# Kernel optimization log

Hardware: AMD Instinct MI355X
Metric: run time of the kernel (lower is better)

## Reference

```python
import jax, jax.numpy as jnp
import numpy as np

NUM_CODES = 1024
CODE_DIM = 256
COMMIT_W = 0.25
EPS = 1e-5
ENT_LO, ENT_HI = 0.5, 0.9
ENT_W = 0.1
VAR_FLOOR = 0.05
VAR_W = 1e-3
DECORR_W = 1e-3


def setup_inputs() -> dict:
    key = jax.random.key(0)
    k1, k2, k3 = jax.random.split(key, 3)
    inputs = jax.random.normal(k1, (16, 2048, CODE_DIM), dtype=jnp.float32)
    weight = jax.random.normal(k2, (NUM_CODES, CODE_DIM), dtype=jnp.float32) * 0.1
    usage_counts = jax.random.uniform(k3, (NUM_CODES,), dtype=jnp.float32)
    return {"inputs": inputs, "weight": weight, "usage_counts": usage_counts}


def reference(inputs, weight, usage_counts):
    K, D = weight.shape
    flat = inputs.reshape(-1, D)  # [N, D]
    # squared euclidean distances [N, K]
    dist = (flat ** 2).sum(axis=1, keepdims=True) - 2.0 * flat @ weight.T + (weight ** 2).sum(axis=1)
    idx = jnp.argmin(dist, axis=1)  # [N]
    quant = weight[idx].reshape(inputs.shape)

    commitment_loss = COMMIT_W * jnp.mean((jax.lax.stop_gradient(quant) - inputs) ** 2)
    # straight-through estimator
    quant_ste = inputs + jax.lax.stop_gradient(quant - inputs)

    # usage entropy regularizer
    probs = usage_counts + EPS
    probs = probs / jnp.maximum(probs.sum(), EPS * K)
    usage_entropy = -jnp.sum(probs * jnp.log(probs + EPS)) / np.log(float(K)).astype(np.float32)
    gap = jnp.where(usage_entropy < ENT_LO, ENT_LO - usage_entropy,
                    jnp.where(usage_entropy > ENT_HI, usage_entropy - ENT_HI, 0.0))
    entropy_loss = ENT_W * gap ** 2

    # variance floor penalty on codebook
    variance = jnp.var(weight, axis=0)
    variance_loss = VAR_W * jnp.mean(jax.nn.relu(VAR_FLOOR - variance))

    # decorrelation penalty
    wc = weight - weight.mean(axis=0, keepdims=True)
    cov = wc.T @ wc / float(K)  # [D, D]
    off_diag = cov - jnp.diag(jnp.diag(cov))
    decorrelation_loss = DECORR_W * jnp.mean(off_diag ** 2)

    total_loss = commitment_loss + entropy_loss + variance_loss + decorrelation_loss
    indices = idx.reshape(inputs.shape[:-1])
    return (quant_ste, indices, total_loss, commitment_loss, entropy_loss,
            variance_loss, decorrelation_loss, usage_entropy)
```

## Files before the change

### kernel.cpp

```cpp
#include <hip/hip_runtime.h>
#include <math.h>

#define DIMS   256
#define KCODES 1024
#define NTOT   32768
#define TAU    4.0e-4f

typedef __bf16 bf16x8 __attribute__((ext_vector_type(8)));
typedef float  f32x4  __attribute__((ext_vector_type(4)));

#define WS_COMMIT   0
#define WS_FLAGCNT  1
#define WS_DECORR   2
#define WS_COLSUM   16
#define WS_COLSQ    272
#define WS_WSQ      1024
#define WS_XSQ      2048
#define WS_FLAGS    34816
#define WS_CAND1    67584
#define WS_CAND2    329728
#define WS_CANDI    591872
#define WS_WP       854016

#define OUT_Q    0
#define OUT_IDX  8388608
#define OUT_SCAL 8421376


__global__ __launch_bounds__(256) void prep_kernel(const float* __restrict__ X,
                                                   const float* __restrict__ W,
                                                   __bf16* __restrict__ Xp,
                                                   __bf16* __restrict__ Wp2,
                                                   float* ws) {
  int b = blockIdx.x;
  int tid = threadIdx.x;
  if (b < 1056) {
    bool isW = b >= 1024;
    const float* src = isW ? W : X;
    __bf16* dst = isW ? Wp2 : Xp;
    int sqoff = isW ? WS_WSQ : WS_XSQ;
    int bb = isW ? b - 1024 : b;
    int kt = tid >> 5, mtl = (tid >> 4) & 1, lc = tid & 15;
    int row = bb * 32 + mtl * 16 + lc;
    int bt = row >> 7, c = row & 127;
    int wv = c >> 6, t = (c >> 4) & 3;
    size_t hibase = ((((size_t)(bt * 8 + kt) * 2 + wv) * 4 + t) * 2) * 512;
    const float* s = src + (size_t)row * DIMS + kt * 32;
    float sq = 0.f;
    #pragma unroll
    for (int kq = 0; kq < 4; kq++) {
      float4 u = *(const float4*)(s + kq * 8);
      float4 v = *(const float4*)(s + kq * 8 + 4);
      float f[8] = {u.x, u.y, u.z, u.w, v.x, v.y, v.z, v.w};
      bf16x8 hi, lo;
      #pragma unroll
      for (int e = 0; e < 8; e++) {
        __bf16 h = (__bf16)f[e];
        hi[e] = h;
        lo[e] = (__bf16)(f[e] - (float)h);
        sq = fmaf(f[e], f[e], sq);
      }
      size_t off = (size_t)(kq * 16 + lc) * 8;
      *(bf16x8*)&dst[hibase + off] = hi;
      *(bf16x8*)&dst[hibase + 512 + off] = lo;
    }
    atomicAdd(&ws[sqoff + row], sq);
  } else if (b < 1064) {
    int d = tid;
    int r0 = (b - 1056) * 128;
    float s = 0.f, sq = 0.f;
    #pragma unroll 8
    for (int k = 0; k < 128; k++) {
      float v = W[(size_t)(r0 + k) * DIMS + d];
      s += v;
      sq = fmaf(v, v, sq);
    }
    atomicAdd(&ws[WS_COLSUM + d], s);
    atomicAdd(&ws[WS_COLSQ + d], sq);
  } else {
    __shared__ float wi_s[2][KCODES];
    __shared__ float red2[256];
    __shared__ float mi_s[2];
    __shared__ float red[4];
    int i0 = (b - 1064) * 2;
    int rr = tid >> 1, cc = tid & 1;
    #pragma unroll
    for (int q = 0; q < 8; q++) {
      int row = q * 128 + rr;
      wi_s[cc][row] = W[(size_t)row * DIMS + i0 + cc];
    }
    __syncthreads();
    float pm = 0.f;
    #pragma unroll
    for (int q = 0; q < 8; q++) pm += wi_s[cc][rr * 8 + q];
    red2[tid] = pm;
    __syncthreads();
    if (tid < 2) {
      float s = 0.f;
      for (int k = tid; k < 256; k += 2) s += red2[k];
      mi_s[tid] = s * (1.0f / 1024.0f);
    }
    int j = tid;
    float a0 = 0.f, a1 = 0.f, sj = 0.f;
    for (int k = 0; k < KCODES; k += 4) {
      #pragma unroll
      for (int u = 0; u < 4; u++) {
        float wj = W[(size_t)(k + u) * DIMS + j];
        a0 = fmaf(wi_s[0][k + u], wj, a0);
        a1 = fmaf(wi_s[1][k + u], wj, a1);
        sj += wj;
      }
    }
    __syncthreads();
    const float inv = 1.0f / 1024.0f;
    float mj = sj * inv;
    float v = 0.f;
    float c0 = a0 * inv - mi_s[0] * mj;
    if (i0 != j) v = fmaf(c0, c0, v);
    float c1 = a1 * inv - mi_s[1] * mj;
    if (i0 + 1 != j) v = fmaf(c1, c1, v);
    #pragma unroll
    for (int m = 32; m >= 1; m >>= 1) v += __shfl_xor(v, m);
    if ((j & 63) == 0) red[j >> 6] = v;
    __syncthreads();
    if (j == 0) atomicAdd(&ws[WS_DECORR], (red[0] + red[1]) + (red[2] + red[3]));
  }
}

__device__ __forceinline__ void stage16(const __bf16* g, __bf16* l) {
  __builtin_amdgcn_global_load_lds(
      (const __attribute__((address_space(1))) void*)g,
      (__attribute__((address_space(3))) void*)l, 16, 0, 0);
}

#define STAGE_PIECE(T, J) do {                                                    \
    int _s = (T) % 3;                                                             \
    if ((J) < 4) {                                                                \
      int _c = (J) >> 1, _h = (J) & 1;                                            \
      stage16(Xp + (size_t)((2 * bm + _c) * 8 + (T)) * 8192 + _h * 4096 + tid * 8,\
              buf + _s * 24576 + _c * 8192 + _h * 4096 + tid * 8);                \
    } else {                                                                      \
      int _h = (J) - 4;                                                           \
      stage16(Wp2 + (size_t)(bn * 8 + (T)) * 8192 + _h * 4096 + tid * 8,          \
              buf + _s * 24576 + 16384 + _h * 4096 + tid * 8);                    \
    }                                                                             \
  } while (0)

__global__ __launch_bounds__(512, 2) void pass1_kernel(const __bf16* __restrict__ Xp,
                                                       const __bf16* __restrict__ Wp2,
                                                       float* ws) {
  __shared__ __align__(16) __bf16 buf[73728];
  __shared__ float wsqs[128];
  __shared__ float d1L[512];
  __shared__ float d2L[512];
  __shared__ int   i1L[512];

  int tid = threadIdx.x;
  int lane = tid & 63, wave = tid >> 6;
  int wm = wave >> 1, wn = wave & 1;
  int quad = lane >> 4, col = lane & 15;
  int l = blockIdx.x;
  int swz = (l & 7) * 128 + (l >> 3);
  int bm = swz >> 3;
  int bn = swz & 7;
  int cb = bn * 128;

  f32x4 acc[4][4];
  #pragma unroll
  for (int i = 0; i < 4; i++)
    #pragma unroll
    for (int j = 0; j < 4; j++) acc[i][j] = (f32x4){0.f, 0.f, 0.f, 0.f};

  wsqs[tid & 127] = ws[WS_WSQ + cb + (tid & 127)];
  asm volatile("" ::: "memory");

  #pragma unroll
  for (int t = 0; t < 3; t++) {
    STAGE_PIECE(t, 0); STAGE_PIECE(t, 1); STAGE_PIECE(t, 2);
    STAGE_PIECE(t, 3); STAGE_PIECE(t, 4); STAGE_PIECE(t, 5);
  }
  asm volatile("s_waitcnt vmcnt(12)" ::: "memory");
  __builtin_amdgcn_s_barrier();

  #pragma unroll
  for (int kt = 0; kt < 8; kt++) {
    const __bf16* bsl = buf + (kt % 3) * 24576 + lane * 8;
    bf16x8 Bf[4][2];
    #pragma unroll
    for (int p = 0; p < 4; p++) {
      bf16x8 A0 = *(const bf16x8*)(bsl + wm * 4096 + (p * 2 + 0) * 512);
      bf16x8 A1 = *(const bf16x8*)(bsl + wm * 4096 + (p * 2 + 1) * 512);
      if (p == 0) {
        #pragma unroll
        for (int nt = 0; nt < 4; nt++) {
          Bf[nt][0] = *(const bf16x8*)(bsl + 16384 + wn * 4096 + (nt * 2 + 0) * 512);
          Bf[nt][1] = *(const bf16x8*)(bsl + 16384 + wn * 4096 + (nt * 2 + 1) * 512);
        }
      }
      if (kt + 2 < 8) {
        if (p == 0) { STAGE_PIECE(kt + 2, 0); STAGE_PIECE(kt + 2, 1); }
        if (p == 1) { STAGE_PIECE(kt + 2, 2); STAGE_PIECE(kt + 2, 3); }
        if (p == 2) { STAGE_PIECE(kt + 2, 4); }
        if (p == 3) { STAGE_PIECE(kt + 2, 5); }
      }
      if (p == 3 && kt < 7) {
        if (kt <= 5) asm volatile("s_waitcnt vmcnt(6)" ::: "memory");
        else         asm volatile("s_waitcnt vmcnt(0)" ::: "memory");
      }
      __builtin_amdgcn_s_barrier();
      asm volatile("s_waitcnt lgkmcnt(0)" ::: "memory");
      __builtin_amdgcn_sched_barrier(0);
      __builtin_amdgcn_s_setprio(1);
      #pragma unroll
      for (int nt = 0; nt < 4; nt++) {
        acc[p][nt] = __builtin_amdgcn_mfma_f32_16x16x32_bf16(A0, Bf[nt][0], acc[p][nt], 0, 0, 0);
        acc[p][nt] = __builtin_amdgcn_mfma_f32_16x16x32_bf16(A0, Bf[nt][1], acc[p][nt], 0, 0, 0);
        acc[p][nt] = __builtin_amdgcn_mfma_f32_16x16x32_bf16(A1, Bf[nt][0], acc[p][nt], 0, 0, 0);
      }
      __builtin_amdgcn_s_setprio(0);
      __builtin_amdgcn_s_barrier();
    }
  }

  #pragma unroll
  for (int mt = 0; mt < 4; mt++) {
    #pragma unroll
    for (int r = 0; r < 4; r++) {
      float d1 = 3.0e38f, d2 = 3.0e38f;
      int i1 = 0;
      #pragma unroll
      for (int nt = 0; nt < 4; nt++) {
        int lc = wn * 64 + nt * 16 + col;
        float d = wsqs[lc] - 2.0f * acc[mt][nt][r];
        int g = cb + lc;
        if (d < d1) { d2 = d1; d1 = d; i1 = g; }
        else if (d < d2) d2 = d;
      }
      #pragma unroll
      for (int m = 1; m < 16; m <<= 1) {
        float od1 = __shfl_xor(d1, m);
        int oi1 = __shfl_xor(i1, m);
        float od2 = __shfl_xor(d2, m);
        if (od1 < d1 || (od1 == d1 && oi1 < i1)) {
          d2 = fminf(d1, fminf(d2, od2));
          d1 = od1; i1 = oi1;
        } else {
          d2 = fminf(od1, fminf(d2, od2));
        }
      }
      if (col == 0) {
        int lr = wm * 64 + mt * 16 + quad * 4 + r;
        d1L[lr * 2 + wn] = d1;
        d2L[lr * 2 + wn] = d2;
        i1L[lr * 2 + wn] = i1;
      }
    }
  }
  __syncthreads();
  if (tid < 256) {
    float a1 = d1L[tid * 2], a2 = d2L[tid * 2];
    int ai = i1L[tid * 2];
    float b1 = d1L[tid * 2 + 1], b2 = d2L[tid * 2 + 1];
    int bi = i1L[tid * 2 + 1];
    float m1, m2; int mi;
    if (b1 < a1 || (b1 == a1 && bi < ai)) { m1 = b1; mi = bi; m2 = fminf(a1, b2); }
    else { m1 = a1; mi = ai; m2 = fminf(b1, a2); }
    int o = bn * NTOT + bm * 256 + tid;
    ws[WS_CAND1 + o] = m1;
    ws[WS_CAND2 + o] = m2;
    ((int*)ws)[WS_CANDI + o] = mi;
  }
}

__global__ __launch_bounds__(256) void pass2_kernel(const float* __restrict__ W,
                                                    float* __restrict__ outQ,
                                                    float* __restrict__ outIdx, float* ws) {
  __shared__ int idx_s[256];
  int tid = threadIdx.x;
  int row = blockIdx.x * 256 + tid;
  const float* c1 = ws + WS_CAND1;
  const float* c2 = ws + WS_CAND2;
  const int* ci = (const int*)ws + WS_CANDI;
  float m1 = 3.0e38f, m2 = 3.0e38f;
  int mi = 0;
  #pragma unroll
  for (int b = 0; b < 8; b++) {
    int o = b * NTOT + row;
    float b1 = c1[o], b2 = c2[o];
    int bi = ci[o];
    if (b1 < m1 || (b1 == m1 && bi < mi)) { m2 = fminf(m1, b2); m1 = b1; mi = bi; }
    else { m2 = fminf(m2, b1); }
  }
  outIdx[row] = (float)mi;
  idx_s[tid] = mi;
  int* wsI = (int*)ws;
  if (m2 - m1 < TAU) {
    int p = atomicAdd(&wsI[WS_FLAGCNT], 1);
    wsI[WS_FLAGS + p] = row;
  }
  float partial = ws[WS_XSQ + row] + m1;
  #pragma unroll
  for (int m = 32; m >= 1; m >>= 1) partial += __shfl_xor(partial, m);
  if ((tid & 63) == 0) atomicAdd(&ws[WS_COMMIT], partial);
  __syncthreads();
  int wave = tid >> 6, lane = tid & 63;
  int rowBase = blockIdx.x * 256;
  #pragma unroll 4
  for (int i = 0; i < 64; i++) {
    int rl = wave * 64 + i;
    int ix = idx_s[rl];
    float4 v = ((const float4*)(W + (size_t)ix * DIMS))[lane];
    ((float4*)(outQ + (size_t)(rowBase + rl) * DIMS))[lane] = v;
  }
}

__global__ __launch_bounds__(256) void refine_kernel(const float* __restrict__ X,
                                                     const float* __restrict__ W,
                                                     float* __restrict__ outQ,
                                                     float* __restrict__ outIdx, float* ws,
                                                     const float* __restrict__ U,
                                                     float* __restrict__ out) {
  __shared__ float xs[DIMS];
  __shared__ double dm[256];
  __shared__ int im[256];
  __shared__ int chosen;
  int tid = threadIdx.x;
  if (blockIdx.x == 512) {
    __shared__ float red[256];
    float s = 0.f;
    for (int e = tid; e < KCODES; e += 256) s += U[e] + 1e-5f;
    red[tid] = s;
    __syncthreads();
    for (int st = 128; st >= 1; st >>= 1) {
      if (tid < st) red[tid] += red[tid + st];
      __syncthreads();
    }
    float S = red[0];
    __syncthreads();
    float denom = fmaxf(S, 1e-5f * 1024.0f);
    float h = 0.f;
    for (int e = tid; e < KCODES; e += 256) {
      float p = (U[e] + 1e-5f) / denom;
      h += p * logf(p + 1e-5f);
    }
    red[tid] = h;
    __syncthreads();
    for (int st = 128; st >= 1; st >>= 1) {
      if (tid < st) red[tid] += red[tid + st];
      __syncthreads();
    }
    float H = -red[0] / 6.93147180559945f;
    __syncthreads();
    float m = ws[WS_COLSUM + tid] * (1.0f / 1024.0f);
    float var = ws[WS_COLSQ + tid] * (1.0f / 1024.0f) - m * m;
    float r = 0.05f - var;
    red[tid] = r > 0.f ? r : 0.f;
    __syncthreads();
    for (int st = 128; st >= 1; st >>= 1) {
      if (tid < st) red[tid] += red[tid + st];
      __syncthreads();
    }
    if (tid == 0) {
      float varloss = 1e-3f * (red[0] / 256.0f);
      float gap = H < 0.5f ? (0.5f - H) : (H > 0.9f ? (H - 0.9f) : 0.0f);
      float entloss = 0.1f * gap * gap;
      float commit = 0.25f * ws[WS_COMMIT] / 8388608.0f;
      float dec = 1e-3f * ws[WS_DECORR] / 65536.0f;
      float* sc = out + OUT_SCAL;
      sc[0] = commit + entloss + varloss + dec;
      sc[1] = commit;
      sc[2] = entloss;
      sc[3] = varloss;
      sc[4] = dec;
      sc[5] = H;
    }
    return;
  }
  const int* wsI = (const int*)ws;
  int cnt = wsI[WS_FLAGCNT];
  const int* list = wsI + WS_FLAGS;
  for (int f = blockIdx.x; f < cnt; f += 512) {
    int row = list[f];
    __syncthreads();
    if (tid < 64) ((float4*)xs)[tid] = ((const float4*)(X + (size_t)row * DIMS))[tid];
    __syncthreads();
    double bd = 1.0e300;
    int bi = 0;
    for (int jj = 0; jj < 4; jj++) {
      int c = tid + 256 * jj;
      double a0 = 0.0, a1 = 0.0, a2 = 0.0, a3 = 0.0;
      const float* wr = W + (size_t)c * DIMS;
      #pragma unroll 4
      for (int d4 = 0; d4 < 64; d4++) {
        float4 w = ((const float4*)wr)[d4];
        float4 x = ((const float4*)xs)[d4];
        double e0 = (double)x.x - (double)w.x;
        double e1 = (double)x.y - (double)w.y;
        double e2 = (double)x.z - (double)w.z;
        double e3 = (double)x.w - (double)w.w;
        a0 += e0 * e0; a1 += e1 * e1; a2 += e2 * e2; a3 += e3 * e3;
      }
      double s = (a0 + a1) + (a2 + a3);
      if (s < bd) { bd = s; bi = c; }
    }
    dm[tid] = bd; im[tid] = bi;
    __syncthreads();
    for (int st = 128; st >= 1; st >>= 1) {
      if (tid < st) {
        if (dm[tid + st] < dm[tid] || (dm[tid + st] == dm[tid] && im[tid + st] < im[tid])) {
          dm[tid] = dm[tid + st]; im[tid] = im[tid + st];
        }
      }
      __syncthreads();
    }
    if (tid == 0) { chosen = im[0]; outIdx[row] = (float)im[0]; }
    __syncthreads();
    int ix = chosen;
    if (tid < 64)
      ((float4*)(outQ + (size_t)row * DIMS))[tid] = ((const float4*)(W + (size_t)ix * DIMS))[tid];
  }
}

extern "C" void kernel_launch(void* const* d_in, const int* in_sizes, int n_in, void* d_out,
                              int out_size, void* d_ws, size_t ws_size, hipStream_t stream) {
  const float* X = (const float*)d_in[0];
  const float* W = (const float*)d_in[1];
  const float* U = (const float*)d_in[2];
  float* out = (float*)d_out;
  float* ws = (float*)d_ws;
  __bf16* Xp = (__bf16*)(out + OUT_Q);
  __bf16* Wp2 = (__bf16*)(ws + WS_WP);

  hipMemsetAsync(d_ws, 0, 139264, stream);
  prep_kernel<<<1192, 256, 0, stream>>>(X, W, Xp, Wp2, ws);
  pass1_kernel<<<1024, 512, 0, stream>>>(Xp, Wp2, ws);
  pass2_kernel<<<NTOT / 256, 256, 0, stream>>>(W, out + OUT_Q, out + OUT_IDX, ws);
  refine_kernel<<<513, 256, 0, stream>>>(X, W, out + OUT_Q, out + OUT_IDX, ws, U, out);
}
```

Baseline: 254.0 us.

## Enlarge pass1 tile to 256 codes and switch to double-buffered staging

Pass1 now gives each workgroup 256 rows by 256 codes instead of 128 codes, so each wave holds twice as many accumulators and the grid shrinks from 1024 to 512 blocks. The aim is to reuse each staged input tile against more codes and so cut global-to-LDS traffic for X. The three-slot LDS pipeline with staggered partial staging becomes a simpler two-slot double buffer with a full wait and barrier each k-step. Pass2 now merges 4 code-block candidates instead of 8. The cost is higher register and LDS pressure, which may lower occupancy, and less overlap between loads and compute.

```diff
diff --git a/kernel.cpp b/kernel.cpp
--- a/kernel.cpp
+++ b/kernel.cpp
@@ -133,97 +133,99 @@
       (__attribute__((address_space(3))) void*)l, 16, 0, 0);
 }
 
-#define STAGE_PIECE(T, J) do {                                                    \
-    int _s = (T) % 3;                                                             \
-    if ((J) < 4) {                                                                \
-      int _c = (J) >> 1, _h = (J) & 1;                                            \
-      stage16(Xp + (size_t)((2 * bm + _c) * 8 + (T)) * 8192 + _h * 4096 + tid * 8,\
-              buf + _s * 24576 + _c * 8192 + _h * 4096 + tid * 8);                \
-    } else {                                                                      \
-      int _h = (J) - 4;                                                           \
-      stage16(Wp2 + (size_t)(bn * 8 + (T)) * 8192 + _h * 4096 + tid * 8,          \
-              buf + _s * 24576 + 16384 + _h * 4096 + tid * 8);                    \
-    }                                                                             \
+#define STAGE_TILE(T) do {                                                          \
+    __bf16* _d = &buf[(T) & 1][0];                                                  \
+    const size_t _tb = (size_t)(T) * 8192;                                          \
+    stage16(Xp + (size_t)(bm * 2 + 0) * 65536 + _tb + 0 * 4096 + tid * 8,           \
+            _d + 0 * 8192 + 0 * 4096 + tid * 8);                                    \
+    stage16(Xp + (size_t)(bm * 2 + 0) * 65536 + _tb + 1 * 4096 + tid * 8,           \
+            _d + 0 * 8192 + 1 * 4096 + tid * 8);                                    \
+    stage16(Xp + (size_t)(bm * 2 + 1) * 65536 + _tb + 0 * 4096 + tid * 8,           \
+            _d + 1 * 8192 + 0 * 4096 + tid * 8);                                    \
+    stage16(Xp + (size_t)(bm * 2 + 1) * 65536 + _tb + 1 * 4096 + tid * 8,           \
+            _d + 1 * 8192 + 1 * 4096 + tid * 8);                                    \
+    stage16(Wp2 + (size_t)(bn * 2 + 0) * 65536 + _tb + 0 * 4096 + tid * 8,          \
+            _d + 16384 + 0 * 8192 + 0 * 4096 + tid * 8);                            \
+    stage16(Wp2 + (size_t)(bn * 2 + 0) * 65536 + _tb + 1 * 4096 + tid * 8,          \
+            _d + 16384 + 0 * 8192 + 1 * 4096 + tid * 8);                            \
+    stage16(Wp2 + (size_t)(bn * 2 + 1) * 65536 + _tb + 0 * 4096 + tid * 8,          \
+            _d + 16384 + 1 * 8192 + 0 * 4096 + tid * 8);                            \
+    stage16(Wp2 + (size_t)(bn * 2 + 1) * 65536 + _tb + 1 * 4096 + tid * 8,          \
+            _d + 16384 + 1 * 8192 + 1 * 4096 + tid * 8);                            \
   } while (0)
 
 __global__ __launch_bounds__(512, 2) void pass1_kernel(const __bf16* __restrict__ Xp,
                                                        const __bf16* __restrict__ Wp2,
                                                        float* ws) {
-  __shared__ __align__(16) __bf16 buf[73728];
-  __shared__ float wsqs[128];
-  __shared__ float d1L[512];
-  __shared__ float d2L[512];
-  __shared__ int   i1L[512];
+  __shared__ __align__(16) __bf16 buf[2][32768];
+  __shared__ float wsqs[256];
+  __shared__ float d1L[256][4];
+  __shared__ float d2L[256][4];
+  __shared__ int   i1L[256][4];
 
   int tid = threadIdx.x;
   int lane = tid & 63, wave = tid >> 6;
-  int wm = wave >> 1, wn = wave & 1;
+  int wm = wave >> 2, wn = wave & 3;
   int quad = lane >> 4, col = lane & 15;
   int l = blockIdx.x;
-  int swz = (l & 7) * 128 + (l >> 3);
-  int bm = swz >> 3;
-  int bn = swz & 7;
-  int cb = bn * 128;
-
-  f32x4 acc[4][4];
+  int swz = (l & 7) * 64 + (l >> 3);
+  int bm = swz >> 2;
+  int bn = swz & 3;
+  int cb = bn * 256;
+
+  f32x4 acc[8][4];
   #pragma unroll
-  for (int i = 0; i < 4; i++)
+  for (int i = 0; i < 8; i++)
     #pragma unroll
     for (int j = 0; j < 4; j++) acc[i][j] = (f32x4){0.f, 0.f, 0.f, 0.f};
 
-  wsqs[tid & 127] = ws[WS_WSQ + cb + (tid & 127)];
+  wsqs[tid & 255] = ws[WS_WSQ + cb + (tid & 255)];
   asm volatile("" ::: "memory");
 
-  #pragma unroll
-  for (int t = 0; t < 3; t++) {
-    STAGE_PIECE(t, 0); STAGE_PIECE(t, 1); STAGE_PIECE(t, 2);
-    STAGE_PIECE(t, 3); STAGE_PIECE(t, 4); STAGE_PIECE(t, 5);
-  }
-  asm volatile("s_waitcnt vmcnt(12)" ::: "memory");
+  STAGE_TILE(0);
+  STAGE_TILE(1);
+  asm volatile("s_waitcnt vmcnt(8)" ::: "memory");
   __builtin_amdgcn_s_barrier();
 
-  #pragma unroll
+  #pragma unroll 2
   for (int kt = 0; kt < 8; kt++) {
-    const __bf16* bsl = buf + (kt % 3) * 24576 + lane * 8;
+    const __bf16* bs = &buf[kt & 1][0];
+    if (kt >= 1 && kt < 7) STAGE_TILE(kt + 1);
     bf16x8 Bf[4][2];
+    const __bf16* bB = bs + 16384 + (wn >> 1) * 8192 + (wn & 1) * 4096 + lane * 8;
+    #pragma unroll
+    for (int nt = 0; nt < 4; nt++) {
+      Bf[nt][0] = *(const bf16x8*)(bB + nt * 1024);
+      Bf[nt][1] = *(const bf16x8*)(bB + nt * 1024 + 512);
+    }
+    const __bf16* bA = bs + wm * 8192 + lane * 8;
     #pragma unroll
     for (int p = 0; p < 4; p++) {
-      bf16x8 A0 = *(const bf16x8*)(bsl + wm * 4096 + (p * 2 + 0) * 512);
-      bf16x8 A1 = *(const bf16x8*)(bsl + wm * 4096 + (p * 2 + 1) * 512);
-      if (p == 0) {
-        #pragma unroll
-        for (int nt = 0; nt < 4; nt++) {
-          Bf[nt][0] = *(const bf16x8*)(bsl + 16384 + wn * 4096 + (nt * 2 + 0) * 512);
-          Bf[nt][1] = *(const bf16x8*)(bsl + 16384 + wn * 4096 + (nt * 2 + 1) * 512);
-        }
-      }
-      if (kt + 2 < 8) {
-        if (p == 0) { STAGE_PIECE(kt + 2, 0); STAGE_PIECE(kt + 2, 1); }
-        if (p == 1) { STAGE_PIECE(kt + 2, 2); STAGE_PIECE(kt + 2, 3); }
-        if (p == 2) { STAGE_PIECE(kt + 2, 4); }
-        if (p == 3) { STAGE_PIECE(kt + 2, 5); }
-      }
-      if (p == 3 && kt < 7) {
-        if (kt <= 5) asm volatile("s_waitcnt vmcnt(6)" ::: "memory");
-        else         asm volatile("s_waitcnt vmcnt(0)" ::: "memory");
-      }
-      __builtin_amdgcn_s_barrier();
-      asm volatile("s_waitcnt lgkmcnt(0)" ::: "memory");
+      bf16x8 A00 = *(const bf16x8*)(bA + (2 * p + 0) * 1024);
+      bf16x8 A01 = *(const bf16x8*)(bA + (2 * p + 0) * 1024 + 512);
+      bf16x8 A10 = *(const bf16x8*)(bA + (2 * p + 1) * 1024);
+      bf16x8 A11 = *(const bf16x8*)(bA + (2 * p + 1) * 1024 + 512);
       __builtin_amdgcn_sched_barrier(0);
       __builtin_amdgcn_s_setprio(1);
       #pragma unroll
       for (int nt = 0; nt < 4; nt++) {
-        acc[p][nt] = __builtin_amdgcn_mfma_f32_16x16x32_bf16(A0, Bf[nt][0], acc[p][nt], 0, 0, 0);
-        acc[p][nt] = __builtin_amdgcn_mfma_f32_16x16x32_bf16(A0, Bf[nt][1], acc[p][nt], 0, 0, 0);
-        acc[p][nt] = __builtin_amdgcn_mfma_f32_16x16x32_bf16(A1, Bf[nt][0], acc[p][nt], 0, 0, 0);
+        acc[2 * p + 0][nt] = __builtin_amdgcn_mfma_f32_16x16x32_bf16(A00, Bf[nt][0], acc[2 * p + 0][nt], 0, 0, 0);
+        acc[2 * p + 0][nt] = __builtin_amdgcn_mfma_f32_16x16x32_bf16(A00, Bf[nt][1], acc[2 * p + 0][nt], 0, 0, 0);
+        acc[2 * p + 0][nt] = __builtin_amdgcn_mfma_f32_16x16x32_bf16(A01, Bf[nt][0], acc[2 * p + 0][nt], 0, 0, 0);
+        acc[2 * p + 1][nt] = __builtin_amdgcn_mfma_f32_16x16x32_bf16(A10, Bf[nt][0], acc[2 * p + 1][nt], 0, 0, 0);
+        acc[2 * p + 1][nt] = __builtin_amdgcn_mfma_f32_16x16x32_bf16(A10, Bf[nt][1], acc[2 * p + 1][nt], 0, 0, 0);
+        acc[2 * p + 1][nt] = __builtin_amdgcn_mfma_f32_16x16x32_bf16(A11, Bf[nt][0], acc[2 * p + 1][nt], 0, 0, 0);
       }
       __builtin_amdgcn_s_setprio(0);
+    }
+    if (kt < 7) {
+      asm volatile("s_waitcnt vmcnt(0)" ::: "memory");
       __builtin_amdgcn_s_barrier();
     }
   }
 
   #pragma unroll
-  for (int mt = 0; mt < 4; mt++) {
+  for (int mt = 0; mt < 8; mt++) {
     #pragma unroll
     for (int r = 0; r < 4; r++) {
       float d1 = 3.0e38f, d2 = 3.0e38f;
@@ -249,22 +251,24 @@
         }
       }
       if (col == 0) {
-        int lr = wm * 64 + mt * 16 + quad * 4 + r;
-        d1L[lr * 2 + wn] = d1;
-        d2L[lr * 2 + wn] = d2;
-        i1L[lr * 2 + wn] = i1;
+        int lr = wm * 128 + mt * 16 + quad * 4 + r;
+        d1L[lr][wn] = d1;
+        d2L[lr][wn] = d2;
+        i1L[lr][wn] = i1;
       }
     }
   }
   __syncthreads();
   if (tid < 256) {
-    float a1 = d1L[tid * 2], a2 = d2L[tid * 2];
-    int ai = i1L[tid * 2];
-    float b1 = d1L[tid * 2 + 1], b2 = d2L[tid * 2 + 1];
-    int bi = i1L[tid * 2 + 1];
-    float m1, m2; int mi;
-    if (b1 < a1 || (b1 == a1 && bi < ai)) { m1 = b1; mi = bi; m2 = fminf(a1, b2); }
-    else { m1 = a1; mi = ai; m2 = fminf(b1, a2); }
+    float m1 = d1L[tid][0], m2 = d2L[tid][0];
+    int mi = i1L[tid][0];
+    #pragma unroll
+    for (int w = 1; w < 4; w++) {
+      float b1 = d1L[tid][w], b2 = d2L[tid][w];
+      int bi = i1L[tid][w];
+      if (b1 < m1 || (b1 == m1 && bi < mi)) { m2 = fminf(m1, b2); m1 = b1; mi = bi; }
+      else { m2 = fminf(m2, fminf(b1, b2)); }
+    }
     int o = bn * NTOT + bm * 256 + tid;
     ws[WS_CAND1 + o] = m1;
     ws[WS_CAND2 + o] = m2;
@@ -284,12 +288,12 @@
   float m1 = 3.0e38f, m2 = 3.0e38f;
   int mi = 0;
   #pragma unroll
-  for (int b = 0; b < 8; b++) {
+  for (int b = 0; b < 4; b++) {
     int o = b * NTOT + row;
     float b1 = c1[o], b2 = c2[o];
     int bi = ci[o];
     if (b1 < m1 || (b1 == m1 && bi < mi)) { m2 = fminf(m1, b2); m1 = b1; mi = bi; }
-    else { m2 = fminf(m2, b1); }
+    else { m2 = fminf(m2, fminf(b1, b2)); }
   }
   outIdx[row] = (float)mi;
   idx_s[tid] = mi;
@@ -433,7 +437,7 @@
 
   hipMemsetAsync(d_ws, 0, 139264, stream);
   prep_kernel<<<1192, 256, 0, stream>>>(X, W, Xp, Wp2, ws);
-  pass1_kernel<<<1024, 512, 0, stream>>>(Xp, Wp2, ws);
+  pass1_kernel<<<512, 512, 0, stream>>>(Xp, Wp2, ws);
   pass2_kernel<<<NTOT / 256, 256, 0, stream>>>(W, out + OUT_Q, out + OUT_IDX, ws);
   refine_kernel<<<513, 256, 0, stream>>>(X, W, out + OUT_Q, out + OUT_IDX, ws, U, out);
 }
```

After: 237.0 us. 6.7% less time.
